# Kernel tuning notes

Measured on AMD Instinct MI355X. Metric: run time of the kernel, lower is better.

The kernel has to match this reference:

```python
import jax, jax.numpy as jnp
import numpy as np

B, T, C = 2, 2048, 1024
H = 16
HD = C // H  # head_dim = 64
SCALE = HD ** -0.5

def setup_inputs() -> dict:
    key = jax.random.key(0)
    ks = jax.random.split(key, 5)
    s = 1.0 / np.sqrt(C)
    return {
        "x": jax.random.normal(ks[0], (B, T, C), dtype=jnp.float32),
        "Wq": jax.random.normal(ks[1], (C, C), dtype=jnp.float32) * s,
        "Wk": jax.random.normal(ks[2], (C, C), dtype=jnp.float32) * s,
        "Wv": jax.random.normal(ks[3], (C, C), dtype=jnp.float32) * s,
        "Wp": jax.random.normal(ks[4], (C, C), dtype=jnp.float32) * s,
        "bp": jnp.zeros((C,), dtype=jnp.float32),
    }

def reference(x, Wq, Wk, Wv, Wp, bp):
    b, t, c = x.shape
    # QKV projections (no bias, qkv_bias=False) -> [B,T,H,HD]
    q = (x @ Wq).reshape(b, t, H, HD)
    k = (x @ Wk).reshape(b, t, H, HD)
    v = (x @ Wv).reshape(b, t, H, HD)
    # scores [B,H,T,T]
    scores = jnp.einsum("bqhd,bkhd->bhqk", q, k) * SCALE
    causal = jnp.tril(jnp.ones((t, t), dtype=bool))
    scores = jnp.where(causal, scores, -jnp.inf)
    attn = jax.nn.softmax(scores, axis=-1)  # dropout = identity (eval mode)
    out = jnp.einsum("bhqk,bkhd->bqhd", attn, v).reshape(b, t, c)
    return out @ Wp + bp
```

## Files before the change

kernel.cpp:

```cpp
#include <hip/hip_runtime.h>


typedef __attribute__((ext_vector_type(8))) short shortx8;
typedef __attribute__((ext_vector_type(4))) short shortx4;
typedef __attribute__((ext_vector_type(8))) unsigned short ushortx8;
typedef __attribute__((ext_vector_type(4))) float f32x4;
typedef __attribute__((ext_vector_type(16))) float f32x16;
typedef __attribute__((ext_vector_type(2))) unsigned uintx2;

#define MFMA16(a, b, c) __builtin_amdgcn_mfma_f32_16x16x32_bf16((a), (b), (c), 0, 0, 0)
#define MFMA32(a, b, c) __builtin_amdgcn_mfma_f32_32x32x16_bf16((a), (b), (c), 0, 0, 0)

#define SC_L2E 0.18033688011112042f

__device__ __forceinline__ unsigned short f2bf(float f) {
  union { float f; unsigned u; } v; v.f = f;
  unsigned r = v.u + 0x7fffu + ((v.u >> 16) & 1u);
  return (unsigned short)(r >> 16);
}

__device__ __forceinline__ unsigned cvtpk(float a, float b) {
  unsigned r;
  asm("v_cvt_pk_bf16_f32 %0, %1, %2" : "=v"(r) : "v"(a), "v"(b));
  return r;
}

__device__ __forceinline__ float fexp2(float x) {
#if __has_builtin(__builtin_amdgcn_exp2f)
  return __builtin_amdgcn_exp2f(x);
#else
  return exp2f(x);
#endif
}

__device__ __forceinline__ uintx2 plswap(unsigned a, unsigned b) {
#if __has_builtin(__builtin_amdgcn_permlane32_swap)
  return __builtin_amdgcn_permlane32_swap(a, b, false, false);
#else
  asm volatile("v_permlane32_swap_b32 %0, %1" : "+v"(a), "+v"(b));
  uintx2 r; r[0] = a; r[1] = b; return r;
#endif
}

__device__ __forceinline__ float partner32(float x, int hi) {
  unsigned u = __builtin_bit_cast(unsigned, x);
  uintx2 r = plswap(u, u);
  return __builtin_bit_cast(float, hi ? r[0] : r[1]);
}

__device__ __forceinline__ void gload16(const void* g, void* l) {
  __builtin_amdgcn_global_load_lds(
      (const __attribute__((address_space(1))) void*)g,
      (__attribute__((address_space(3))) void*)l, 16, 0, 0);
}

__global__ __launch_bounds__(256) void cvt_x(const float* __restrict__ x,
                                             unsigned short* __restrict__ xb, int n4) {
  int i = blockIdx.x * 256 + threadIdx.x;
  if (i < n4) {
    float4 v = ((const float4*)x)[i];
    unsigned short* o = xb + (size_t)i * 4;
    o[0] = f2bf(v.x); o[1] = f2bf(v.y); o[2] = f2bf(v.z); o[3] = f2bf(v.w);
  }
}

__global__ __launch_bounds__(256) void transpose_w4(
    const float* __restrict__ Wq, const float* __restrict__ Wk,
    const float* __restrict__ Wv, const float* __restrict__ Wp,
    unsigned short* __restrict__ wqkvT, unsigned short* __restrict__ wpT) {
  __shared__ float tile[32][33];
  const int zi = blockIdx.z;
  const float* src = (zi == 0) ? Wq : (zi == 1) ? Wk : (zi == 2) ? Wv : Wp;
  unsigned short* dst = (zi == 3) ? wpT : wqkvT + (size_t)zi * 1048576;
  const int bx = blockIdx.x * 32, by = blockIdx.y * 32;
  const int tx = threadIdx.x & 31, ty = threadIdx.x >> 5;
  #pragma unroll
  for (int i = 0; i < 32; i += 8)
    tile[ty + i][tx] = src[(size_t)(by + ty + i) * 1024 + bx + tx];
  __syncthreads();
  #pragma unroll
  for (int i = 0; i < 32; i += 8)
    dst[(size_t)(bx + ty + i) * 1024 + by + tx] = f2bf(tile[tx][ty + i]);
}

__global__ __launch_bounds__(256) void gemm_bt(
    const unsigned short* __restrict__ A, const unsigned short* __restrict__ BT,
    unsigned short* __restrict__ Cb, float* __restrict__ Cf,
    const float* __restrict__ bias, int M, int N, int K,
    float qscale, int scale_cols, unsigned short* __restrict__ vTo) {
  __shared__ unsigned short As[3][4096];
  __shared__ unsigned short Bs[3][4096];
  const int tid = threadIdx.x;
  const int lane = tid & 63, w = tid >> 6;
  const int wr = w >> 1, wc = w & 1;
  const int brow = blockIdx.y << 7, bcol = blockIdx.x << 7;

  f32x4 z = {0.f, 0.f, 0.f, 0.f};
  f32x4 acc[4][4];
  #pragma unroll
  for (int m = 0; m < 4; ++m)
    #pragma unroll
    for (int n = 0; n < 4; ++n) acc[m][n] = z;

  const int srow = tid >> 2;
  const int scol = (tid & 3) << 3;
  const unsigned short* Ap = A + (size_t)(brow + srow) * K + scol;
  const unsigned short* Bp = BT + (size_t)(bcol + srow) * K + scol;
  const size_t rowK64 = (size_t)64 * K;

  #define GSTAGE(k0_, bi_)                                   \
    do {                                                     \
      unsigned short* AsW = &As[bi_][w * 512];               \
      unsigned short* BsW = &Bs[bi_][w * 512];               \
      gload16(Ap + (k0_), AsW);                              \
      gload16(Ap + rowK64 + (k0_), AsW + 2048);              \
      gload16(Bp + (k0_), BsW);                              \
      gload16(Bp + rowK64 + (k0_), BsW + 2048);              \
    } while (0)

  const int koff = (lane >> 4) << 3;
  const int ar = (wr << 6) + (lane & 15);
  const int br = (wc << 6) + (lane & 15);
  const int nt = K >> 5;
  int cur = 0, sb = 2;
  GSTAGE(0, 0);
  GSTAGE(32, 1);
  for (int t = 0; t < nt; ++t) {
    if (t + 2 < nt) {
      GSTAGE((size_t)(t + 2) << 5, sb);
      sb = (sb == 2) ? 0 : sb + 1;
      asm volatile("s_waitcnt vmcnt(8)" ::: "memory");
    } else if (t + 1 < nt) {
      asm volatile("s_waitcnt vmcnt(4)" ::: "memory");
    } else {
      asm volatile("s_waitcnt vmcnt(0)" ::: "memory");
    }
    __builtin_amdgcn_sched_barrier(0);
    __builtin_amdgcn_s_barrier();
    __builtin_amdgcn_sched_barrier(0);
    shortx8 af[4], bf[4];
    #pragma unroll
    for (int m = 0; m < 4; ++m) af[m] = *(const shortx8*)&As[cur][(ar + m * 16) * 32 + koff];
    #pragma unroll
    for (int n = 0; n < 4; ++n) bf[n] = *(const shortx8*)&Bs[cur][(br + n * 16) * 32 + koff];
    #pragma unroll
    for (int m = 0; m < 4; ++m)
      #pragma unroll
      for (int n = 0; n < 4; ++n) acc[m][n] = MFMA16(af[m], bf[n], acc[m][n]);
    asm volatile("s_waitcnt lgkmcnt(0)" ::: "memory");
    __builtin_amdgcn_sched_barrier(0);
    __builtin_amdgcn_s_barrier();
    __builtin_amdgcn_sched_barrier(0);
    cur = (cur == 2) ? 0 : cur + 1;
  }
  #undef GSTAGE

  const int r0 = (lane >> 4) << 2;
  const int c0 = lane & 15;
  if (Cb) {
    if (vTo && bcol >= 2048) {
      #pragma unroll
      for (int m = 0; m < 4; ++m)
        #pragma unroll
        for (int n = 0; n < 4; ++n) {
          const int dp = bcol - 2048 + (wc << 6) + n * 16 + c0;
          const size_t rowb = brow + (wr << 6) + m * 16 + r0;
          uint2 u;
          u.x = cvtpk(acc[m][n][0], acc[m][n][1]);
          u.y = cvtpk(acc[m][n][2], acc[m][n][3]);
          *(uint2*)&vTo[(size_t)dp * 4096 + rowb] = u;
        }
    } else {
      #pragma unroll
      for (int m = 0; m < 4; ++m)
        #pragma unroll
        for (int n = 0; n < 4; ++n)
          #pragma unroll
          for (int j = 0; j < 4; ++j) {
            const size_t row = brow + (wr << 6) + m * 16 + r0 + j;
            const size_t col = bcol + (wc << 6) + n * 16 + c0;
            float v = acc[m][n][j];
            if ((int)col < scale_cols) v *= qscale;
            Cb[row * N + col] = f2bf(v);
          }
    }
  } else {
    #pragma unroll
    for (int m = 0; m < 4; ++m)
      #pragma unroll
      for (int n = 0; n < 4; ++n)
        #pragma unroll
        for (int j = 0; j < 4; ++j) {
          const size_t row = brow + (wr << 6) + m * 16 + r0 + j;
          const size_t col = bcol + (wc << 6) + n * 16 + c0;
          Cf[row * N + col] = acc[m][n][j] + bias[col];
        }
  }
}


__global__ __launch_bounds__(256, 4) void attn_fwd(
    const unsigned short* __restrict__ qkv, const unsigned short* __restrict__ vT,
    unsigned short* __restrict__ att) {
  __shared__ unsigned short sh[4][4096];

  const int tid = threadIdx.x;
  const int lane = tid & 63;
  const int p = tid >> 6;
  const int stream = blockIdx.x;
  const int h = stream & 15, b = stream >> 4;
  const int qb = 63 - (int)blockIdx.y;
  const int ql = lane & 31;
  const int hi = lane >> 5;
  const int q = qb * 32 + ql;

  shortx8 qf[4];
  {
    const unsigned short* qp = qkv + ((size_t)(b * 2048 + q)) * 3072 + h * 64 + 8 * hi;
    #pragma unroll
    for (int kc = 0; kc < 4; ++kc) qf[kc] = *(const shortx8*)(qp + 16 * kc);
  }

  f32x16 z16;
  #pragma unroll
  for (int i = 0; i < 16; ++i) z16[i] = 0.f;
  f32x16 accO0 = z16, accO1 = z16;
  float m_run = -__builtin_inff(), l_run = 0.f;

  const unsigned short* kb[4];
  const unsigned short* vb[4];
  #pragma unroll
  for (int i = 0; i < 4; ++i) {
    const int krow = 8 * i + (lane >> 3);
    const int kcl = (lane & 7) ^ (((krow >> 1) ^ (krow >> 4)) & 7);
    kb[i] = qkv + ((size_t)(b * 2048 + krow)) * 3072 + 1024 + h * 64 + 8 * kcl;
    const int vrow = 16 * i + (lane >> 2);
    const int vcl = (lane & 3) ^ (((vrow >> 1) ^ (vrow >> 3)) & 3);
    vb[i] = vT + ((size_t)(h * 64 + vrow)) * 4096 + b * 2048 + 8 * vcl;
  }
  const int rs8 = ((ql >> 1) ^ (ql >> 4)) & 7;
  const int rs4 = ((ql >> 1) ^ (ql >> 3)) & 3;

  unsigned short* Kl = &sh[p][0];
  unsigned short* Vl = &sh[p][2048];

  #define STAGE(t_)                                                        \
    do {                                                                   \
      _Pragma("unroll")                                                    \
      for (int i = 0; i < 4; ++i) {                                        \
        gload16(kb[i] + (size_t)(t_) * 32 * 3072, Kl + i * 512);           \
        gload16(vb[i] + (t_) * 32, Vl + i * 512);                          \
      }                                                                    \
    } while (0)

  if (p <= qb) STAGE(p);
  for (int t = p; t <= qb; t += 4) {
    asm volatile("s_waitcnt vmcnt(0)" ::: "memory");
    __builtin_amdgcn_sched_barrier(0);

    shortx8 kf[4];
    #pragma unroll
    for (int kc = 0; kc < 4; ++kc)
      kf[kc] = *(const shortx8*)&Kl[ql * 64 + 8 * ((2 * kc + hi) ^ rs8)];
    shortx8 vf[2][2];
    #pragma unroll
    for (int dh = 0; dh < 2; ++dh)
      #pragma unroll
      for (int ks = 0; ks < 2; ++ks)
        vf[dh][ks] = *(const shortx8*)&Vl[(32 * dh + ql) * 32 + 8 * ((2 * ks + hi) ^ rs4)];
    asm volatile("s_waitcnt lgkmcnt(0)" ::: "memory");
    __builtin_amdgcn_sched_barrier(0);

    if (t + 4 <= qb) STAGE(t + 4);

    __builtin_amdgcn_s_setprio(1);
    f32x16 s = z16;
    #pragma unroll
    for (int kc = 0; kc < 4; ++kc) s = MFMA32(kf[kc], qf[kc], s);
    __builtin_amdgcn_s_setprio(0);

    if (t == qb) {
      #pragma unroll
      for (int r = 0; r < 16; ++r) {
        const int kvl = (r & 3) + 8 * (r >> 2) + 4 * hi;
        if (kvl > ql) s[r] = -__builtin_inff();
      }
    }

    float m8[8], m4[4];
    #pragma unroll
    for (int i = 0; i < 8; ++i) m8[i] = fmaxf(s[2 * i], s[2 * i + 1]);
    #pragma unroll
    for (int i = 0; i < 4; ++i) m4[i] = fmaxf(m8[2 * i], m8[2 * i + 1]);
    float mx = fmaxf(fmaxf(m4[0], m4[1]), fmaxf(m4[2], m4[3]));
    mx = fmaxf(mx, partner32(mx, hi));

    if (!__all(mx <= m_run + 8.0f)) {
      const float nm = fmaxf(m_run, mx);
      const float alpha = fexp2(m_run - nm);
      l_run *= alpha;
      #pragma unroll
      for (int r = 0; r < 16; ++r) { accO0[r] *= alpha; accO1[r] *= alpha; }
      m_run = nm;
    }

    #pragma unroll
    for (int r = 0; r < 16; ++r) s[r] = fexp2(s[r] - m_run);
    float a8[8], a4[4];
    #pragma unroll
    for (int i = 0; i < 8; ++i) a8[i] = s[2 * i] + s[2 * i + 1];
    #pragma unroll
    for (int i = 0; i < 4; ++i) a4[i] = a8[2 * i] + a8[2 * i + 1];
    float rsum = (a4[0] + a4[1]) + (a4[2] + a4[3]);
    rsum += partner32(rsum, hi);
    l_run += rsum;

    unsigned wv[8];
    #pragma unroll
    for (int i = 0; i < 8; ++i) wv[i] = cvtpk(s[2 * i], s[2 * i + 1]);
    __builtin_amdgcn_s_setprio(1);
    #pragma unroll
    for (int ss = 0; ss < 2; ++ss) {
      uintx2 r02 = plswap(wv[4 * ss], wv[4 * ss + 2]);
      uintx2 r13 = plswap(wv[4 * ss + 1], wv[4 * ss + 3]);
      union { unsigned u[4]; shortx8 s8; } pb;
      pb.u[0] = r02[0];
      pb.u[1] = r13[0];
      pb.u[2] = r02[1];
      pb.u[3] = r13[1];
      accO0 = MFMA32(vf[0][ss], pb.s8, accO0);
      accO1 = MFMA32(vf[1][ss], pb.s8, accO1);
    }
    __builtin_amdgcn_s_setprio(0);
  }
  #undef STAGE

  float* fb = (float*)&sh[0][0];
  #define DUMP(slot_)                                                          \
    do {                                                                       \
      float* ob = fb + (slot_) * 2048;                                         \
      _Pragma("unroll")                                                        \
      for (int rg = 0; rg < 4; ++rg) {                                         \
        f32x4 v0 = {accO0[4 * rg], accO0[4 * rg + 1],                          \
                    accO0[4 * rg + 2], accO0[4 * rg + 3]};                     \
        f32x4 v1 = {accO1[4 * rg], accO1[4 * rg + 1],                          \
                    accO1[4 * rg + 2], accO1[4 * rg + 3]};                     \
        *(f32x4*)&ob[(rg * 64 + lane) * 4] = v0;                               \
        *(f32x4*)&ob[((4 + rg) * 64 + lane) * 4] = v1;                         \
      }                                                                        \
      fb[4096 + (slot_) * 128 + lane] = m_run;                                 \
      fb[4096 + (slot_) * 128 + 64 + lane] = l_run;                            \
    } while (0)
  #define MERGE(slot_)                                                         \
    do {                                                                       \
      const float m2 = fb[4096 + (slot_) * 128 + lane];                        \
      const float l2 = fb[4096 + (slot_) * 128 + 64 + lane];                   \
      if (m2 != -__builtin_inff()) {                                           \
        float* ob = fb + (slot_) * 2048;                                       \
        const float mf = fmaxf(m_run, m2);                                     \
        const float a1 = fexp2(m_run - mf);                                    \
        const float a2 = fexp2(m2 - mf);                                       \
        _Pragma("unroll")                                                      \
        for (int rg = 0; rg < 4; ++rg) {                                       \
          f32x4 p0 = *(const f32x4*)&ob[(rg * 64 + lane) * 4];                 \
          f32x4 p1 = *(const f32x4*)&ob[((4 + rg) * 64 + lane) * 4];           \
          _Pragma("unroll")                                                    \
          for (int j = 0; j < 4; ++j) {                                        \
            accO0[4 * rg + j] = accO0[4 * rg + j] * a1 + p0[j] * a2;           \
            accO1[4 * rg + j] = accO1[4 * rg + j] * a1 + p1[j] * a2;           \
          }                                                                    \
        }                                                                      \
        l_run = l_run * a1 + l2 * a2;                                          \
        m_run = mf;                                                            \
      }                                                                        \
    } while (0)

  __syncthreads();
  if (p == 1) DUMP(0);
  if (p == 3) DUMP(1);
  __syncthreads();
  if (p == 0) MERGE(0);
  if (p == 2) MERGE(1);
  __syncthreads();
  if (p == 2) DUMP(0);
  __syncthreads();
  if (p == 0) {
    MERGE(0);
    const float inv = 1.f / l_run;
    unsigned short* op = att + ((size_t)(b * 2048 + q)) * 1024 + h * 64;
    #pragma unroll
    for (int rq = 0; rq < 4; ++rq) {
      shortx4 o0, o1;
      #pragma unroll
      for (int j = 0; j < 4; ++j) {
        o0[j] = (short)f2bf(accO0[4 * rq + j] * inv);
        o1[j] = (short)f2bf(accO1[4 * rq + j] * inv);
      }
      *(shortx4*)&op[8 * rq + 4 * hi] = o0;
      *(shortx4*)&op[32 + 8 * rq + 4 * hi] = o1;
    }
  }
  #undef DUMP
  #undef MERGE
}

extern "C" void kernel_launch(void* const* d_in, const int* in_sizes, int n_in,
                              void* d_out, int out_size, void* d_ws, size_t ws_size,
                              hipStream_t stream) {
  const float* x  = (const float*)d_in[0];
  const float* Wq = (const float*)d_in[1];
  const float* Wk = (const float*)d_in[2];
  const float* Wv = (const float*)d_in[3];
  const float* Wp = (const float*)d_in[4];
  const float* bp = (const float*)d_in[5];

  char* ws = (char*)d_ws;
  unsigned short* xb    = (unsigned short*)(ws);
  unsigned short* wqkvT = (unsigned short*)(ws + (size_t)8  * 1048576);
  unsigned short* wpT   = (unsigned short*)(ws + (size_t)14 * 1048576);
  unsigned short* qkv   = (unsigned short*)(ws + (size_t)16 * 1048576);
  unsigned short* vT    = (unsigned short*)(ws + (size_t)40 * 1048576);
  unsigned short* att   = (unsigned short*)(ws + (size_t)48 * 1048576);

  cvt_x<<<dim3(4096), dim3(256), 0, stream>>>(x, xb, 1048576);
  transpose_w4<<<dim3(32, 32, 4), dim3(256), 0, stream>>>(Wq, Wk, Wv, Wp, wqkvT, wpT);
  gemm_bt<<<dim3(24, 32), dim3(256), 0, stream>>>(xb, wqkvT, qkv, nullptr, nullptr,
                                                  4096, 3072, 1024, SC_L2E, 1024, vT);
  attn_fwd<<<dim3(32, 64), dim3(256), 0, stream>>>(qkv, vT, att);
  gemm_bt<<<dim3(8, 32), dim3(256), 0, stream>>>(att, wpT, nullptr, (float*)d_out, bp,
                                                 4096, 1024, 1024, 0.f, 0, nullptr);
}
```

Measured before the change: 111.5 us.

## Reduce GEMM pipeline depth, drop trailing barrier, split K/V waits in attention

```diff
diff --git a/kernel.cpp b/kernel.cpp
--- a/kernel.cpp
+++ b/kernel.cpp
@@ -46,6 +46,10 @@
   unsigned u = __builtin_bit_cast(unsigned, x);
   uintx2 r = plswap(u, u);
   return __builtin_bit_cast(float, hi ? r[0] : r[1]);
+}
+
+__device__ __forceinline__ float max3(float a, float b, float c) {
+  return fmaxf(fmaxf(a, b), c);
 }
 
 __device__ __forceinline__ void gload16(const void* g, void* l) {
@@ -122,15 +126,12 @@
   const int ar = (wr << 6) + (lane & 15);
   const int br = (wc << 6) + (lane & 15);
   const int nt = K >> 5;
-  int cur = 0, sb = 2;
+  int cur = 0;
   GSTAGE(0, 0);
-  GSTAGE(32, 1);
   for (int t = 0; t < nt; ++t) {
-    if (t + 2 < nt) {
-      GSTAGE((size_t)(t + 2) << 5, sb);
-      sb = (sb == 2) ? 0 : sb + 1;
-      asm volatile("s_waitcnt vmcnt(8)" ::: "memory");
-    } else if (t + 1 < nt) {
+    const int nxt = (cur + 1 == 3) ? 0 : cur + 1;
+    if (t + 1 < nt) {
+      GSTAGE((size_t)(t + 1) << 5, nxt);
       asm volatile("s_waitcnt vmcnt(4)" ::: "memory");
     } else {
       asm volatile("s_waitcnt vmcnt(0)" ::: "memory");
@@ -149,9 +150,7 @@
       for (int n = 0; n < 4; ++n) acc[m][n] = MFMA16(af[m], bf[n], acc[m][n]);
     asm volatile("s_waitcnt lgkmcnt(0)" ::: "memory");
     __builtin_amdgcn_sched_barrier(0);
-    __builtin_amdgcn_s_barrier();
-    __builtin_amdgcn_sched_barrier(0);
-    cur = (cur == 2) ? 0 : cur + 1;
+    cur = nxt;
   }
   #undef GSTAGE
 
@@ -247,21 +246,32 @@
   #define STAGE(t_)                                                        \
     do {                                                                   \
       _Pragma("unroll")                                                    \
-      for (int i = 0; i < 4; ++i) {                                        \
+      for (int i = 0; i < 4; ++i)                                          \
         gload16(kb[i] + (size_t)(t_) * 32 * 3072, Kl + i * 512);           \
+      _Pragma("unroll")                                                    \
+      for (int i = 0; i < 4; ++i)                                          \
         gload16(vb[i] + (t_) * 32, Vl + i * 512);                          \
-      }                                                                    \
     } while (0)
 
   if (p <= qb) STAGE(p);
   for (int t = p; t <= qb; t += 4) {
-    asm volatile("s_waitcnt vmcnt(0)" ::: "memory");
-    __builtin_amdgcn_sched_barrier(0);
-
+    asm volatile("s_waitcnt vmcnt(4)" ::: "memory");
+    __builtin_amdgcn_sched_barrier(0);
     shortx8 kf[4];
     #pragma unroll
     for (int kc = 0; kc < 4; ++kc)
       kf[kc] = *(const shortx8*)&Kl[ql * 64 + 8 * ((2 * kc + hi) ^ rs8)];
+    asm volatile("s_waitcnt lgkmcnt(0)" ::: "memory");
+    __builtin_amdgcn_sched_barrier(0);
+
+    __builtin_amdgcn_s_setprio(1);
+    f32x16 s = z16;
+    #pragma unroll
+    for (int kc = 0; kc < 4; ++kc) s = MFMA32(kf[kc], qf[kc], s);
+    __builtin_amdgcn_s_setprio(0);
+
+    asm volatile("s_waitcnt vmcnt(0)" ::: "memory");
+    __builtin_amdgcn_sched_barrier(0);
     shortx8 vf[2][2];
     #pragma unroll
     for (int dh = 0; dh < 2; ++dh)
@@ -272,12 +282,6 @@
     __builtin_amdgcn_sched_barrier(0);
 
     if (t + 4 <= qb) STAGE(t + 4);
-
-    __builtin_amdgcn_s_setprio(1);
-    f32x16 s = z16;
-    #pragma unroll
-    for (int kc = 0; kc < 4; ++kc) s = MFMA32(kf[kc], qf[kc], s);
-    __builtin_amdgcn_s_setprio(0);
 
     if (t == qb) {
       #pragma unroll
@@ -287,12 +291,12 @@
       }
     }
 
-    float m8[8], m4[4];
-    #pragma unroll
-    for (int i = 0; i < 8; ++i) m8[i] = fmaxf(s[2 * i], s[2 * i + 1]);
-    #pragma unroll
-    for (int i = 0; i < 4; ++i) m4[i] = fmaxf(m8[2 * i], m8[2 * i + 1]);
-    float mx = fmaxf(fmaxf(m4[0], m4[1]), fmaxf(m4[2], m4[3]));
+    float t0 = max3(s[0], s[1], s[2]);
+    float t1 = max3(s[3], s[4], s[5]);
+    float t2 = max3(s[6], s[7], s[8]);
+    float t3 = max3(s[9], s[10], s[11]);
+    float t4 = max3(s[12], s[13], s[14]);
+    float mx = fmaxf(max3(t0, t1, t2), max3(t3, t4, s[15]));
     mx = fmaxf(mx, partner32(mx, hi));
 
     if (!__all(mx <= m_run + 8.0f)) {
```

New measurement: 107.8 us (median of 3 runs). 3.3% less time.
